# Optimization experiments

Hardware: AMD Instinct MI355X
Metric: run time of the kernel (lower is better)

The kernel has to match this reference:

```python
import jax, jax.numpy as jnp
import numpy as np

B, N, FP, TP = 4, 64, 256, 32
V, D = 32000, 1024


def setup_inputs() -> dict:
    key = jax.random.key(0)
    k1, k2, k3 = jax.random.split(key, 3)
    x_prime = jax.random.normal(k1, (B, N, FP, TP), dtype=jnp.float32)
    token_embedding = jax.random.normal(k2, (V, D), dtype=jnp.float32) * 0.02
    # xavier_uniform for W: bound = sqrt(6/(F'+V))
    bound = np.sqrt(6.0 / (FP + V)).astype(np.float32)
    W = jax.random.uniform(k3, (FP, V), dtype=jnp.float32, minval=-bound, maxval=bound)
    b = jnp.zeros((V,), dtype=jnp.float32)
    return {"x_prime": x_prime, "token_embedding": token_embedding, "W": W, "b": b}


def reference(x_prime, token_embedding, W, b):
    # x_prime: (B, N, F', T') -> permute(0,3,1,2) -> (B, T', N, F') -> (B, L, F'), L = N*T'
    Bb, Nn, Fp, Tp = x_prime.shape
    x_flat = jnp.transpose(x_prime, (0, 3, 1, 2)).reshape(Bb, Nn * Tp, Fp)
    # logits: (B, L, V); temperature == 1.0 so no division
    logits = jnp.einsum('blf,fv->blv', x_flat, W) + b
    P = jax.nn.softmax(logits, axis=-1)          # (B, L, V)
    H_graph = jnp.einsum('blv,vd->bld', P, token_embedding)  # (B, L, d_model)
    return H_graph
```

## Files before the change

### kernel.cpp

```cpp
#include <hip/hip_runtime.h>
#include <cstdint>
#include <cstddef>

typedef __bf16 bf16_t;
typedef __bf16 bf16x8 __attribute__((ext_vector_type(8)));
typedef float f32x4 __attribute__((ext_vector_type(4)));

#define B_  4
#define N_  64
#define FP_ 256
#define TP_ 32
#define V_  32000
#define D_  1024
#define L_  2048
#define M_  8192
#define VT_ 125

__device__ __forceinline__ void async_copy16(const void* g, void* l) {
  __builtin_amdgcn_global_load_lds(
      (__attribute__((address_space(1))) void*)g,
      (__attribute__((address_space(3))) void*)l,
      16, 0, 0);
}

__global__ __launch_bounds__(256) void k_convert_x(const float* __restrict__ xp,
                                                   bf16_t* __restrict__ Xb) {
  __shared__ float tile[256][33];
  const int tid = threadIdx.x;
  const int b = blockIdx.x >> 6;
  const int n = blockIdx.x & 63;
  const float* src = xp + (size_t)(b * N_ + n) * FP_ * TP_;
#pragma unroll
  for (int i = 0; i < 32; i++) {
    int idx = i * 256 + tid;
    tile[idx >> 5][idx & 31] = src[idx];
  }
  __syncthreads();
#pragma unroll
  for (int t = 0; t < 32; t++) {
    Xb[(size_t)(b * L_ + t * N_ + n) * FP_ + tid] = (bf16_t)tile[tid][t];
  }
}

__global__ void k_transpose_cvt(const float* __restrict__ src, bf16_t* __restrict__ dst,
                                int R, int C) {
  __shared__ float tile[64][65];
  int ct = blockIdx.x;
  int rt = blockIdx.y;
  int tid = threadIdx.x;
#pragma unroll
  for (int i = 0; i < 16; i++) {
    int idx = tid + i * 256;
    int a = idx >> 6, bc = idx & 63;
    tile[a][bc] = src[(size_t)(rt * 64 + a) * C + ct * 64 + bc];
  }
  __syncthreads();
#pragma unroll
  for (int i = 0; i < 16; i++) {
    int idx = tid + i * 256;
    int a = idx >> 6, bc = idx & 63;
    dst[(size_t)(ct * 64 + a) * R + rt * 64 + bc] = (bf16_t)tile[bc][a];
  }
}

#define BAR() asm volatile("s_barrier" ::: "memory")
#define VMW(n) asm volatile("s_waitcnt vmcnt(" #n ")" ::: "memory")

__global__ __launch_bounds__(512, 4) void k_gemm1(
    const bf16_t* __restrict__ Xb, const bf16_t* __restrict__ Wt,
    const float* __restrict__ bias, bf16_t* __restrict__ P,
    float* __restrict__ rs_part, int mbase) {
  __shared__ __align__(16) bf16_t smem[36864];

  const int tid = threadIdx.x;
  const int lane = tid & 63;
  const int wid = tid >> 6;
  const int wm = wid >> 2;
  const int wn = wid & 3;
  const int c16 = lane & 15, quad = lane >> 4;

  const int nwg = (int)gridDim.x;
  const int q = nwg >> 3, r = nwg & 7;
  const int xcd = blockIdx.x & 7, bidx = (int)blockIdx.x >> 3;
  const int vb = (xcd < r) ? xcd * (q + 1) + bidx : r + xcd * q + bidx;
  const int vtile = vb % VT_;
  const int mtile = vb / VT_;

  const int v0 = vtile * 256;
  const int prow0 = mtile * 128;
  const int m0 = mbase + prow0;

  const int l3 = lane >> 3;
  const int cA = (lane & 7) ^ l3;
  const int grA = (l3 << 1) + (cA >> 2);
  const int gcA = (cA & 3) << 3;

  const bf16_t* srcA  = Xb + (size_t)(m0 + wid * 16 + grA) * FP_ + gcA;
  const bf16_t* srcB0 = Wt + (size_t)(v0 + (wid * 2 + 0) * 16 + grA) * FP_ + gcA;
  const bf16_t* srcB1 = Wt + (size_t)(v0 + (wid * 2 + 1) * 16 + grA) * FP_ + gcA;
  const int ofsA  = wid * 512;
  const int ofsB0 = (wid * 2 + 0) * 512;
  const int ofsB1 = (wid * 2 + 1) * 512;

  float bv[4];
#pragma unroll
  for (int J = 0; J < 4; J++)
    bv[J] = bias[v0 + wn * 64 + J * 16 + c16];

  f32x4 acc[4][4];
#pragma unroll
  for (int i = 0; i < 4; i++)
#pragma unroll
    for (int j = 0; j < 4; j++) acc[i][j] = (f32x4){0.f, 0.f, 0.f, 0.f};

#define G1_STAGE(buf, t)                                                  \
  do {                                                                    \
    async_copy16(srcA  + (t) * 32, &smem[(buf) * 12288 + ofsA]);          \
    async_copy16(srcB0 + (t) * 32, &smem[(buf) * 12288 + 4096 + ofsB0]);  \
    async_copy16(srcB1 + (t) * 32, &smem[(buf) * 12288 + 4096 + ofsB1]);  \
  } while (0)

  G1_STAGE(0, 0);
  G1_STAGE(1, 1);
  VMW(0);
  BAR();

  const int NT = FP_ >> 5;
  int cur = 0;
  for (int t = 0; t < NT; ++t) {
    if (t > 0) {
      if (t < NT - 1) VMW(3);
      else            VMW(0);
      BAR();
    }
    const int nx2 = (cur == 0) ? 2 : cur - 1;
    if (t < NT - 2) G1_STAGE(nx2, t + 2);

    const int bo = cur * 12288;
    bf16x8 bfr[4];
#pragma unroll
    for (int j = 0; j < 4; j++) {
      int rn = wn * 64 + j * 16 + c16;
      int pn = rn >> 1;
      int cz = (((rn & 1) << 2) | quad) ^ (pn & 7);
      bfr[j] = *(const bf16x8*)&smem[bo + 4096 + pn * 64 + (cz << 3)];
    }
    __builtin_amdgcn_s_setprio(1);
#pragma unroll
    for (int i = 0; i < 4; i++) {
      int rr = wm * 64 + i * 16 + c16;
      int pa = rr >> 1;
      int cz = (((rr & 1) << 2) | quad) ^ (pa & 7);
      bf16x8 a = *(const bf16x8*)&smem[bo + pa * 64 + (cz << 3)];
#pragma unroll
      for (int j = 0; j < 4; j++)
        acc[i][j] = __builtin_amdgcn_mfma_f32_16x16x32_bf16(a, bfr[j], acc[i][j], 0, 0, 0);
    }
    __builtin_amdgcn_s_setprio(0);
    cur = (cur == 2) ? 0 : cur + 1;
  }

#pragma unroll
  for (int I = 0; I < 4; I++) {
    int rowb = wm * 64 + I * 16;
#pragma unroll
    for (int e = 0; e < 4; e++) {
      int row = rowb + quad * 4 + e;
      float s = 0.0f;
#pragma unroll
      for (int J = 0; J < 4; J++) {
        float p = __expf(acc[I][J][e] + bv[J]);
        float pf32 = (float)(bf16_t)p;
        acc[I][J][e] = pf32;
        s += pf32;
      }
#pragma unroll
      for (int off = 1; off < 16; off <<= 1) s += __shfl_xor(s, off, 16);
      if (c16 == 0)
        rs_part[(size_t)(prow0 + row) * 512 + vtile * 4 + wn] = s;
    }
  }

  __syncthreads();
#pragma unroll
  for (int I = 0; I < 4; I++) {
    int rowb = wm * 64 + I * 16;
#pragma unroll
    for (int e = 0; e < 4; e++) {
      int row = rowb + quad * 4 + e;
#pragma unroll
      for (int J = 0; J < 4; J++) {
        int ch = wn * 8 + J * 2 + (c16 >> 3);
        smem[row * 256 + ((ch ^ (row & 7)) << 3) + (c16 & 7)] = (bf16_t)acc[I][J][e];
      }
    }
  }
  __syncthreads();
#pragma unroll
  for (int it = 0; it < 8; it++) {
    int idx2 = it * 512 + tid;
    int row = idx2 >> 5, ch = idx2 & 31;
    *(bf16x8*)&P[(size_t)(prow0 + row) * V_ + v0 + ch * 8] =
        *(const bf16x8*)&smem[row * 256 + ((ch ^ (row & 7)) << 3)];
  }
#undef G1_STAGE
}

__global__ void k_rowsum_reduce(const float* __restrict__ rs_part,
                                float* __restrict__ rowsum, int mbase) {
  int row = blockIdx.x * 4 + (threadIdx.x >> 6);
  int lane = threadIdx.x & 63;
  float s = 0.0f;
  for (int j = lane; j < VT_ * 4; j += 64) s += rs_part[(size_t)row * 512 + j];
#pragma unroll
  for (int off = 32; off >= 1; off >>= 1) s += __shfl_xor(s, off, 64);
  if (lane == 0) rowsum[mbase + row] = s;
}

__global__ __launch_bounds__(512, 4) void k_gemm2(
    const bf16_t* __restrict__ P, const bf16_t* __restrict__ Et,
    float* __restrict__ partial, int mtiles, int chunkrows, int kper) {
  __shared__ __align__(16) bf16_t lds[3][12288];

  const int tid = threadIdx.x;
  const int lane = tid & 63;
  const int wid = tid >> 6;
  const int wm = wid >> 2;
  const int wn = wid & 3;
  const int c16 = lane & 15, quad = lane >> 4;

  const int nwg = (int)gridDim.x;
  const int xcd = blockIdx.x & 7;
  const int vb = xcd * (nwg >> 3) + ((int)blockIdx.x >> 3);
  const int dtile = vb & 3;
  const int rest = vb >> 2;
  const int mtile = rest % mtiles;
  const int kslice = rest / mtiles;

  const int d0 = dtile * 256;
  const int prow0 = mtile * 128;
  const int kbase = kslice * kper;
  float* __restrict__ o = partial + (size_t)kslice * chunkrows * D_;

  const int l3 = lane >> 3;
  const int cA = (lane & 7) ^ l3;
  const int grA = (l3 << 1) + (cA >> 2);
  const int gcA = (cA & 3) << 3;

  const bf16_t* srcA  = P  + (size_t)(prow0 + wid * 16 + grA) * V_ + kbase + gcA;
  const bf16_t* srcB0 = Et + (size_t)(d0 + (wid * 2 + 0) * 16 + grA) * V_ + kbase + gcA;
  const bf16_t* srcB1 = Et + (size_t)(d0 + (wid * 2 + 1) * 16 + grA) * V_ + kbase + gcA;
  const int ofsA  = wid * 512;
  const int ofsB0 = (wid * 2 + 0) * 512;
  const int ofsB1 = (wid * 2 + 1) * 512;

  f32x4 acc[4][4];
#pragma unroll
  for (int i = 0; i < 4; i++)
#pragma unroll
    for (int j = 0; j < 4; j++) acc[i][j] = (f32x4){0.f, 0.f, 0.f, 0.f};

#define G2_STAGE(buf, t)                                                \
  do {                                                                  \
    async_copy16(srcA  + (size_t)(t) * 32, &lds[buf][ofsA]);            \
    async_copy16(srcB0 + (size_t)(t) * 32, &lds[buf][4096 + ofsB0]);    \
    async_copy16(srcB1 + (size_t)(t) * 32, &lds[buf][4096 + ofsB1]);    \
  } while (0)

  G2_STAGE(0, 0);
  G2_STAGE(1, 1);
  VMW(0);
  BAR();

  const int NT = kper >> 5;
  int cur = 0;
  for (int t = 0; t < NT; ++t) {
    if (t > 0) {
      if (t < NT - 1) VMW(3);
      else            VMW(0);
      BAR();
    }
    const int nx2 = (cur == 0) ? 2 : cur - 1;
    if (t < NT - 2) G2_STAGE(nx2, t + 2);

    bf16x8 bfr[4];
#pragma unroll
    for (int j = 0; j < 4; j++) {
      int rn = wn * 64 + j * 16 + c16;
      int pn = rn >> 1;
      int cz = (((rn & 1) << 2) | quad) ^ (pn & 7);
      bfr[j] = *(const bf16x8*)&lds[cur][4096 + pn * 64 + (cz << 3)];
    }
    __builtin_amdgcn_s_setprio(1);
#pragma unroll
    for (int i = 0; i < 4; i++) {
      int rr = wm * 64 + i * 16 + c16;
      int pa = rr >> 1;
      int cz = (((rr & 1) << 2) | quad) ^ (pa & 7);
      bf16x8 a = *(const bf16x8*)&lds[cur][pa * 64 + (cz << 3)];
#pragma unroll
      for (int j = 0; j < 4; j++)
        acc[i][j] = __builtin_amdgcn_mfma_f32_16x16x32_bf16(a, bfr[j], acc[i][j], 0, 0, 0);
    }
    __builtin_amdgcn_s_setprio(0);
    cur = (cur == 2) ? 0 : cur + 1;
  }

#pragma unroll
  for (int i = 0; i < 4; i++) {
#pragma unroll
    for (int e = 0; e < 4; e++) {
      int pr = prow0 + wm * 64 + i * 16 + quad * 4 + e;
#pragma unroll
      for (int j = 0; j < 4; j++) {
        int d = d0 + wn * 64 + j * 16 + c16;
        o[(size_t)pr * D_ + d] = acc[i][j][e];
      }
    }
  }
#undef G2_STAGE
}

#undef BAR
#undef VMW

__global__ void k_finalize(const float* __restrict__ partial,
                           const float* __restrict__ rowsum, float* __restrict__ out,
                           int mbase, int rows, int ks) {
  int i = blockIdx.x * 256 + threadIdx.x;
  int lr = i >> 8;
  float inv = 1.0f / rowsum[mbase + lr];
  f32x4 s = (f32x4){0.f, 0.f, 0.f, 0.f};
  for (int z = 0; z < ks; z++) {
    f32x4 a = ((const f32x4*)(partial + (size_t)z * rows * D_))[i];
    s.x += a.x; s.y += a.y; s.z += a.z; s.w += a.w;
  }
  s.x *= inv; s.y *= inv; s.z *= inv; s.w *= inv;
  ((f32x4*)out)[(size_t)mbase * (D_ / 4) + i] = s;
}

extern "C" void kernel_launch(void* const* d_in, const int* in_sizes, int n_in,
                              void* d_out, int out_size, void* d_ws, size_t ws_size,
                              hipStream_t stream) {
  const float* xp   = (const float*)d_in[0];
  const float* E    = (const float*)d_in[1];
  const float* W    = (const float*)d_in[2];
  const float* bias = (const float*)d_in[3];
  float* out = (float*)d_out;

  char* ws = (char*)d_ws;
  const size_t szXb = (size_t)M_ * FP_ * 2;
  const size_t szWt = (size_t)V_ * FP_ * 2;
  const size_t szEt = (size_t)D_ * V_ * 2;
  const size_t szRs = (size_t)M_ * 4;
  bf16_t* Xb = (bf16_t*)ws;
  bf16_t* Wt = (bf16_t*)(ws + szXb);
  bf16_t* Et = (bf16_t*)(ws + szXb + szWt);
  float* rowsum = (float*)(ws + szXb + szWt + szEt);
  const size_t fixed = szXb + szWt + szEt + szRs;

  const int copt[4] = {8192, 4096, 2048, 1024};
  const int kopt[4] = {2, 4, 8, 16};
  int chunk = 1024, ksv = 16;
  size_t avail = (ws_size > fixed) ? ws_size - fixed : 0;
  for (int i = 0; i < 4; i++) {
    size_t need = (size_t)copt[i] * V_ * 2 + (size_t)kopt[i] * copt[i] * D_ * 4
                + (size_t)copt[i] * 512 * 4;
    if (need <= avail) { chunk = copt[i]; ksv = kopt[i]; break; }
  }
  bf16_t* P = (bf16_t*)(ws + fixed);
  float* partial = (float*)(ws + fixed + (size_t)chunk * V_ * 2);
  float* rs_part = (float*)(ws + fixed + (size_t)chunk * V_ * 2
                            + (size_t)ksv * chunk * D_ * 4);
  const int kper = V_ / ksv;

  k_convert_x<<<B_ * N_, 256, 0, stream>>>(xp, Xb);
  {
    dim3 g(V_ / 64, FP_ / 64);
    k_transpose_cvt<<<g, 256, 0, stream>>>(W, Wt, FP_, V_);
  }
  {
    dim3 g(D_ / 64, V_ / 64);
    k_transpose_cvt<<<g, 256, 0, stream>>>(E, Et, V_, D_);
  }

  for (int mb = 0; mb < M_; mb += chunk) {
    int rows = M_ - mb;
    if (rows > chunk) rows = chunk;

    int nwg1 = VT_ * (rows / 128);
    k_gemm1<<<nwg1, 512, 0, stream>>>(Xb, Wt, bias, P, rs_part, mb);
    k_rowsum_reduce<<<rows / 4, 256, 0, stream>>>(rs_part, rowsum, mb);

    int mt = rows / 128;
    int nwg2 = 4 * mt * ksv;
    k_gemm2<<<nwg2, 512, 0, stream>>>(P, Et, partial, mt, rows, kper);

    k_finalize<<<rows, 256, 0, stream>>>(partial, rowsum, out, mb, rows, ksv);
  }
}
```

Measured before the change: 1.109 ms.

## Enlarge gemm2 tile to 256x256 with K-step 64 and double buffering

The P·E GEMM kernel now computes 256-row by 256-column output tiles. Each wave holds 8x4 MFMA accumulators and each pipeline stage loads a 64-wide K slab, replacing 128x256 tiles with 32-wide K and triple buffering. The goal is better operand reuse and fewer barriers per unit of MFMA work. The split-K choices move from 8/16 to 10/20 slices to keep enough workgroups at the smaller chunk sizes. The cost is 128KB of LDS per block, which limits occupancy to about one block per CU. Going from three buffers to two also leaves less room to hide load latency.

After: 1.064 ms. 4.0% less time.

```diff
diff --git a/kernel.cpp b/kernel.cpp
--- a/kernel.cpp
+++ b/kernel.cpp
@@ -217,10 +217,10 @@
   if (lane == 0) rowsum[mbase + row] = s;
 }
 
-__global__ __launch_bounds__(512, 4) void k_gemm2(
+__global__ __launch_bounds__(512, 2) void k_gemm2(
     const bf16_t* __restrict__ P, const bf16_t* __restrict__ Et,
     float* __restrict__ partial, int mtiles, int chunkrows, int kper) {
-  __shared__ __align__(16) bf16_t lds[3][12288];
+  __shared__ __align__(16) bf16_t lds[2][32768];
 
   const int tid = threadIdx.x;
   const int lane = tid & 63;
@@ -238,7 +238,7 @@
   const int kslice = rest / mtiles;
 
   const int d0 = dtile * 256;
-  const int prow0 = mtile * 128;
+  const int prow0 = mtile * 256;
   const int kbase = kslice * kper;
   float* __restrict__ o = partial + (size_t)kslice * chunkrows * D_;
 
@@ -247,70 +247,81 @@
   const int grA = (l3 << 1) + (cA >> 2);
   const int gcA = (cA & 3) << 3;
 
-  const bf16_t* srcA  = P  + (size_t)(prow0 + wid * 16 + grA) * V_ + kbase + gcA;
-  const bf16_t* srcB0 = Et + (size_t)(d0 + (wid * 2 + 0) * 16 + grA) * V_ + kbase + gcA;
-  const bf16_t* srcB1 = Et + (size_t)(d0 + (wid * 2 + 1) * 16 + grA) * V_ + kbase + gcA;
-  const int ofsA  = wid * 512;
-  const int ofsB0 = (wid * 2 + 0) * 512;
-  const int ofsB1 = (wid * 2 + 1) * 512;
-
-  f32x4 acc[4][4];
-#pragma unroll
-  for (int i = 0; i < 4; i++)
+  const bf16_t* srcA0 = P  + (size_t)(prow0 + (wid * 2 + 0) * 16 + grA) * V_ + kbase + gcA;
+  const bf16_t* srcA1 = P  + (size_t)(prow0 + (wid * 2 + 1) * 16 + grA) * V_ + kbase + gcA;
+  const bf16_t* srcB0 = Et + (size_t)(d0   + (wid * 2 + 0) * 16 + grA) * V_ + kbase + gcA;
+  const bf16_t* srcB1 = Et + (size_t)(d0   + (wid * 2 + 1) * 16 + grA) * V_ + kbase + gcA;
+  const int ofs0 = (wid * 2 + 0) * 512;
+  const int ofs1 = (wid * 2 + 1) * 512;
+
+  f32x4 acc[8][4];
+#pragma unroll
+  for (int i = 0; i < 8; i++)
 #pragma unroll
     for (int j = 0; j < 4; j++) acc[i][j] = (f32x4){0.f, 0.f, 0.f, 0.f};
 
 #define G2_STAGE(buf, t)                                                \
   do {                                                                  \
-    async_copy16(srcA  + (size_t)(t) * 32, &lds[buf][ofsA]);            \
-    async_copy16(srcB0 + (size_t)(t) * 32, &lds[buf][4096 + ofsB0]);    \
-    async_copy16(srcB1 + (size_t)(t) * 32, &lds[buf][4096 + ofsB1]);    \
+    const bf16_t* a0_ = srcA0 + (size_t)(t) * 64;                       \
+    const bf16_t* a1_ = srcA1 + (size_t)(t) * 64;                       \
+    const bf16_t* b0_ = srcB0 + (size_t)(t) * 64;                       \
+    const bf16_t* b1_ = srcB1 + (size_t)(t) * 64;                       \
+    async_copy16(a0_,      &lds[buf][ofs0]);                            \
+    async_copy16(a0_ + 32, &lds[buf][8192 + ofs0]);                     \
+    async_copy16(a1_,      &lds[buf][ofs1]);                            \
+    async_copy16(a1_ + 32, &lds[buf][8192 + ofs1]);                     \
+    async_copy16(b0_,      &lds[buf][16384 + ofs0]);                    \
+    async_copy16(b0_ + 32, &lds[buf][24576 + ofs0]);                    \
+    async_copy16(b1_,      &lds[buf][16384 + ofs1]);                    \
+    async_copy16(b1_ + 32, &lds[buf][24576 + ofs1]);                    \
   } while (0)
 
   G2_STAGE(0, 0);
-  G2_STAGE(1, 1);
   VMW(0);
   BAR();
 
-  const int NT = kper >> 5;
-  int cur = 0;
+  const int NT = kper >> 6;
   for (int t = 0; t < NT; ++t) {
-    if (t > 0) {
-      if (t < NT - 1) VMW(3);
-      else            VMW(0);
+    const int cur = t & 1, nb = cur ^ 1;
+    const bool pf = (t + 1 < NT);
+    if (pf) G2_STAGE(nb, t + 1);
+
+#pragma unroll
+    for (int kk = 0; kk < 2; kk++) {
+      const int ko = kk * 8192;
+      bf16x8 bfr[4];
+#pragma unroll
+      for (int j = 0; j < 4; j++) {
+        int rn = wn * 64 + j * 16 + c16;
+        int pn = rn >> 1;
+        int cz = (((rn & 1) << 2) | quad) ^ (pn & 7);
+        bfr[j] = *(const bf16x8*)&lds[cur][16384 + ko + pn * 64 + (cz << 3)];
+      }
+      __builtin_amdgcn_s_setprio(1);
+#pragma unroll
+      for (int i = 0; i < 8; i++) {
+        int rr = wm * 128 + i * 16 + c16;
+        int pa = rr >> 1;
+        int cz = (((rr & 1) << 2) | quad) ^ (pa & 7);
+        bf16x8 a = *(const bf16x8*)&lds[cur][ko + pa * 64 + (cz << 3)];
+#pragma unroll
+        for (int j = 0; j < 4; j++)
+          acc[i][j] = __builtin_amdgcn_mfma_f32_16x16x32_bf16(a, bfr[j], acc[i][j], 0, 0, 0);
+      }
+      __builtin_amdgcn_s_setprio(0);
+    }
+
+    if (pf) {
+      VMW(0);
       BAR();
     }
-    const int nx2 = (cur == 0) ? 2 : cur - 1;
-    if (t < NT - 2) G2_STAGE(nx2, t + 2);
-
-    bf16x8 bfr[4];
-#pragma unroll
-    for (int j = 0; j < 4; j++) {
-      int rn = wn * 64 + j * 16 + c16;
-      int pn = rn >> 1;
-      int cz = (((rn & 1) << 2) | quad) ^ (pn & 7);
-      bfr[j] = *(const bf16x8*)&lds[cur][4096 + pn * 64 + (cz << 3)];
-    }
-    __builtin_amdgcn_s_setprio(1);
-#pragma unroll
-    for (int i = 0; i < 4; i++) {
-      int rr = wm * 64 + i * 16 + c16;
-      int pa = rr >> 1;
-      int cz = (((rr & 1) << 2) | quad) ^ (pa & 7);
-      bf16x8 a = *(const bf16x8*)&lds[cur][pa * 64 + (cz << 3)];
-#pragma unroll
-      for (int j = 0; j < 4; j++)
-        acc[i][j] = __builtin_amdgcn_mfma_f32_16x16x32_bf16(a, bfr[j], acc[i][j], 0, 0, 0);
-    }
-    __builtin_amdgcn_s_setprio(0);
-    cur = (cur == 2) ? 0 : cur + 1;
-  }
-
-#pragma unroll
-  for (int i = 0; i < 4; i++) {
+  }
+
+#pragma unroll
+  for (int i = 0; i < 8; i++) {
 #pragma unroll
     for (int e = 0; e < 4; e++) {
-      int pr = prow0 + wm * 64 + i * 16 + quad * 4 + e;
+      int pr = prow0 + wm * 128 + i * 16 + quad * 4 + e;
 #pragma unroll
       for (int j = 0; j < 4; j++) {
         int d = d0 + wn * 64 + j * 16 + c16;
@@ -360,8 +371,8 @@
   const size_t fixed = szXb + szWt + szEt + szRs;
 
   const int copt[4] = {8192, 4096, 2048, 1024};
-  const int kopt[4] = {2, 4, 8, 16};
-  int chunk = 1024, ksv = 16;
+  const int kopt[4] = {2, 4, 10, 20};
+  int chunk = 1024, ksv = 20;
   size_t avail = (ws_size > fixed) ? ws_size - fixed : 0;
   for (int i = 0; i < 4; i++) {
     size_t need = (size_t)copt[i] * V_ * 2 + (size_t)kopt[i] * copt[i] * D_ * 4
@@ -392,9 +403,9 @@
     k_gemm1<<<nwg1, 512, 0, stream>>>(Xb, Wt, bias, P, rs_part, mb);
     k_rowsum_reduce<<<rows / 4, 256, 0, stream>>>(rs_part, rowsum, mb);
 
-    int mt = rows / 128;
-    int nwg2 = 4 * mt * ksv;
-    k_gemm2<<<nwg2, 512, 0, stream>>>(P, Et, partial, mt, rows, kper);
+    int mt2 = rows / 256;
+    int nwg2 = 4 * mt2 * ksv;
+    k_gemm2<<<nwg2, 512, 0, stream>>>(P, Et, partial, mt2, rows, kper);
 
     k_finalize<<<rows, 256, 0, stream>>>(partial, rowsum, out, mb, rows, ksv);
   }
```
